# Kernel tuning notes

Measured on AMD Instinct MI355X. Metric: run time of the kernel, lower is better.

The kernel has to match this reference:

```python
import jax, jax.numpy as jnp
import numpy as np

B, T, H = 128, 2048, 128

def setup_inputs() -> dict:
    key = jax.random.key(0)
    k1, k2, k3, k4, k5, k6 = jax.random.split(key, 6)
    s = 1.0 / np.sqrt(H)
    return {
        "H_pos": jax.random.normal(k1, (B, T, H), jnp.float32),
        "H_dyn": jax.random.normal(k2, (B, T, H), jnp.float32),
        "acc_w": jax.random.uniform(k3, (B, T), jnp.float32),
        "W_h": jax.random.uniform(k4, (H, H), jnp.float32, -s, s),
        "W_d": jax.random.uniform(k5, (H, H), jnp.float32, -s, s),
        "W_a": jax.random.uniform(k6, (H,), jnp.float32, -s, s),
        "b_a": jnp.zeros((), jnp.float32),
        "beta": jnp.zeros((), jnp.float32),
    }

def reference(H_pos, H_dyn, acc_w, W_h, W_d, W_a, b_a, beta):
    # energy: W_a(tanh(W_h H_pos + W_d H_dyn)) -> [B, T]
    z = jnp.tanh(jnp.einsum('bth,oh->bto', H_pos, W_h)
                 + jnp.einsum('bth,oh->bto', H_dyn, W_d))
    energy = jnp.einsum('bth,h->bt', z, W_a) + b_a
    # acceleration normalization
    acc_norm = acc_w / jnp.clip(jnp.max(acc_w, axis=1, keepdims=True), 1e-6)
    beta_pos = jax.nn.softplus(beta)
    alpha = jax.nn.softmax(energy * (1.0 + beta_pos * acc_norm), axis=1)  # [B, T]
    context = jnp.einsum('bt,bth->bh', alpha, H_pos)  # [B, H]
    return (context, alpha)
```

## Files before the change

### kernel.cpp

```cpp
#include <hip/hip_runtime.h>

#define B_ 128
#define T_ 2048
#define H_ 128

typedef __attribute__((ext_vector_type(8))) short short8;
typedef __attribute__((ext_vector_type(4))) float f32x4;

__device__ __forceinline__ unsigned short f2b(float f) {
    unsigned int u = __float_as_uint(f);
    u += 0x7fffu + ((u >> 16) & 1u);
    return (unsigned short)(u >> 16);
}
__device__ __forceinline__ short8 pack8(const float4 x, const float4 y) {
    short8 r;
    r[0] = (short)f2b(x.x); r[1] = (short)f2b(x.y);
    r[2] = (short)f2b(x.z); r[3] = (short)f2b(x.w);
    r[4] = (short)f2b(y.x); r[5] = (short)f2b(y.y);
    r[6] = (short)f2b(y.z); r[7] = (short)f2b(y.w);
    return r;
}
__device__ __forceinline__ float tanh_fast(float x) {
    x = fminf(fmaxf(x, -20.f), 20.f);
    float e = __expf(2.f * x);
    return (e - 1.f) / (e + 1.f);
}

__global__ __launch_bounds__(256) void amax_kernel(
    const float* __restrict__ accw, float* __restrict__ amax_g)
{
    __shared__ float wred[4];
    const int b = blockIdx.x, tid = threadIdx.x;
    const float* p = accw + (size_t)b * T_ + tid * 8;
    float4 a0 = *(const float4*)p, a1 = *(const float4*)(p + 4);
    float m = fmaxf(fmaxf(fmaxf(a0.x, a0.y), fmaxf(a0.z, a0.w)),
                    fmaxf(fmaxf(a1.x, a1.y), fmaxf(a1.z, a1.w)));
    for (int d = 32; d >= 1; d >>= 1) m = fmaxf(m, __shfl_xor(m, d, 64));
    if ((tid & 63) == 0) wred[tid >> 6] = m;
    __syncthreads();
    if (tid == 0)
        amax_g[b] = fmaxf(fmaxf(wred[0], wred[1]), fmaxf(wred[2], wred[3]));
}

__global__ __launch_bounds__(512) void energy_kernel(
    const float* __restrict__ Hp,
    const float* __restrict__ Hd,
    const float* __restrict__ accw,
    const float* __restrict__ Wh,
    const float* __restrict__ Wd,
    const float* __restrict__ Wa,
    const float* __restrict__ ba_p,
    const float* __restrict__ beta_p,
    const float* __restrict__ amax_g,
    float* __restrict__ s_g,
    float* __restrict__ ml_g,
    float* __restrict__ ctxp_g,
    int ntiles)
{
    __shared__ unsigned short Wpack[8 * 8 * 64 * 8];
    __shared__ float Was[H_];
    __shared__ float e_s[128];
    __shared__ float s_s[128];
    __shared__ float p_s[128];
    __shared__ float red[16 * H_];
    __shared__ float mld[2];

    const int tid = threadIdx.x;

    for (int i = tid; i < (H_ * H_) / 4; i += 512) {
        int o  = i >> 5;
        int c4 = i & 31;
        float4 wh = *(const float4*)&Wh[o * H_ + c4 * 4];
        float4 wd = *(const float4*)&Wd[o * H_ + c4 * 4];
        uint2 ph, pdv;
        ph.x  = (unsigned)f2b(wh.x) | ((unsigned)f2b(wh.y) << 16);
        ph.y  = (unsigned)f2b(wh.z) | ((unsigned)f2b(wh.w) << 16);
        pdv.x = (unsigned)f2b(wd.x) | ((unsigned)f2b(wd.y) << 16);
        pdv.y = (unsigned)f2b(wd.z) | ((unsigned)f2b(wd.w) << 16);
        int nt   = o >> 4;
        int l15o = o & 15;
        int kth  = c4 >> 3;
        int lq   = (c4 >> 1) & 3;
        int half = (c4 & 1) * 4;
        int bh = ((kth * 8 + nt) * 64 + lq * 16 + l15o) * 8 + half;
        int bd = (((kth + 4) * 8 + nt) * 64 + lq * 16 + l15o) * 8 + half;
        *(uint2*)&Wpack[bh] = ph;
        *(uint2*)&Wpack[bd] = pdv;
    }
    if (tid < H_) Was[tid] = Wa[tid];
    __syncthreads();

    const float ba = ba_p[0];
    const float beta_pos = log1pf(__expf(beta_p[0]));

    const int wave = tid >> 6;
    const int lane = tid & 63;
    const int l15  = lane & 15;
    const int lq   = lane >> 4;

    const unsigned short* wb = Wpack + lane * 8;

    const size_t estep = (size_t)gridDim.x * 128 * H_;

    const int row0 = blockIdx.x * 128 + wave * 16;
    const float* pp = Hp + (size_t)(row0 + l15) * H_ + lq * 8;
    const float* pd = Hd + (size_t)(row0 + l15) * H_ + lq * 8;

    float4 abuf[8];
    #pragma unroll
    for (int c = 0; c < 4; c++) {
        abuf[2 * c]     = *(const float4*)(pp + c * 32);
        abuf[2 * c + 1] = *(const float4*)(pp + c * 32 + 4);
    }

    for (int tile = blockIdx.x; tile < ntiles; tile += gridDim.x) {
        __syncthreads();

        const int b  = tile >> 4;
        const int t0 = (tile & 15) * 128;
        const size_t adv = (tile + (int)gridDim.x < ntiles) ? estep : 0;
        const float* ppn = pp + adv;

        f32x4 acc[8];
        #pragma unroll
        for (int nt = 0; nt < 8; nt++) acc[nt] = (f32x4){0.f, 0.f, 0.f, 0.f};

        #pragma unroll
        for (int kt = 0; kt < 8; kt++) {
            const int sl = kt & 3;
            short8 af = pack8(abuf[2 * sl], abuf[2 * sl + 1]);
            const float* s = (kt < 4) ? (pd + kt * 32) : (ppn + (kt - 4) * 32);
            abuf[2 * sl]     = *(const float4*)s;
            abuf[2 * sl + 1] = *(const float4*)(s + 4);
            #pragma unroll
            for (int nt = 0; nt < 8; nt++) {
                short8 bf = *(const short8*)(wb + kt * 4096 + nt * 512);
                acc[nt] = __builtin_amdgcn_mfma_f32_16x16x32_bf16(af, bf, acc[nt], 0, 0, 0);
            }
            __builtin_amdgcn_sched_barrier(0);
        }
        pp = ppn;
        pd += adv;

        float ep[4] = {0.f, 0.f, 0.f, 0.f};
        #pragma unroll
        for (int nt = 0; nt < 8; nt++) {
            const float wa = Was[nt * 16 + l15];
            #pragma unroll
            for (int r = 0; r < 4; r++) ep[r] += tanh_fast(acc[nt][r]) * wa;
        }
        #pragma unroll
        for (int m = 1; m < 16; m <<= 1) {
            #pragma unroll
            for (int r = 0; r < 4; r++) ep[r] += __shfl_xor(ep[r], m, 64);
        }
        if (l15 == 0) {
            #pragma unroll
            for (int r = 0; r < 4; r++)
                e_s[wave * 16 + lq * 4 + r] = ep[r] + ba;
        }
        __syncthreads();

        if (tid < 128) {
            float a = accw[(size_t)b * T_ + t0 + tid];
            float invd = beta_pos / fmaxf(amax_g[b], 1e-6f);
            float s = e_s[tid] * (1.f + a * invd);
            s_s[tid] = s;
            s_g[(size_t)b * T_ + t0 + tid] = s;
        }
        __syncthreads();

        if (wave == 0) {
            float m = fmaxf(s_s[lane], s_s[lane + 64]);
            for (int d = 32; d >= 1; d >>= 1) m = fmaxf(m, __shfl_xor(m, d, 64));
            if (lane == 0) mld[0] = m;
        }
        __syncthreads();
        const float mt = mld[0];
        if (tid < 128) p_s[tid] = __expf(s_s[tid] - mt);
        __syncthreads();

        if (wave == 0) {
            float l = p_s[lane] + p_s[lane + 64];
            for (int d = 32; d >= 1; d >>= 1) l += __shfl_xor(l, d, 64);
            if (lane == 0) {
                ml_g[(b * 16 + (tile & 15)) * 2 + 0] = mt;
                ml_g[(b * 16 + (tile & 15)) * 2 + 1] = l;
            }
        }

        {
            const int g  = tid >> 5;
            const int c4 = tid & 31;
            const float* base = Hp + ((size_t)b * T_ + t0) * H_ + c4 * 4;
            float c0 = 0.f, c1 = 0.f, c2 = 0.f, c3 = 0.f;
            #pragma unroll
            for (int r = 0; r < 8; r++) {
                int t = r * 16 + g;
                float pv = p_s[t];
                float4 v = *(const float4*)(base + (size_t)t * H_);
                c0 += pv * v.x; c1 += pv * v.y; c2 += pv * v.z; c3 += pv * v.w;
            }
            red[g * H_ + c4 * 4 + 0] = c0;
            red[g * H_ + c4 * 4 + 1] = c1;
            red[g * H_ + c4 * 4 + 2] = c2;
            red[g * H_ + c4 * 4 + 3] = c3;
        }
        __syncthreads();
        if (tid < 128) {
            float s = 0.f;
            #pragma unroll
            for (int g = 0; g < 16; g++) s += red[g * H_ + tid];
            ctxp_g[((size_t)b * 16 + (tile & 15)) * H_ + tid] = s;
        }
    }
}

__global__ __launch_bounds__(256) void combine_kernel(
    const float* __restrict__ s_g,
    const float* __restrict__ ml_g,
    const float* __restrict__ ctxp_g,
    float* __restrict__ out_ctx,
    float* __restrict__ out_alpha)
{
    __shared__ float ml_s[32];
    const int b = blockIdx.x, tid = threadIdx.x;

    if (tid < 32) ml_s[tid] = ml_g[b * 32 + tid];
    __syncthreads();

    float M = -1e30f;
    #pragma unroll
    for (int i = 0; i < 16; i++) M = fmaxf(M, ml_s[2 * i]);
    float L = 0.f;
    #pragma unroll
    for (int i = 0; i < 16; i++) L += __expf(ml_s[2 * i] - M) * ml_s[2 * i + 1];
    const float invL = 1.f / L;

    if (tid < 128) {
        float s = 0.f;
        #pragma unroll
        for (int ti = 0; ti < 16; ti++)
            s += __expf(ml_s[2 * ti] - M) * ctxp_g[((size_t)b * 16 + ti) * H_ + tid];
        out_ctx[b * H_ + tid] = s * invL;
    }

    const float* ps = s_g + (size_t)b * T_ + tid * 8;
    float* pa = out_alpha + (size_t)b * T_ + tid * 8;
    float4 s0 = *(const float4*)ps, s1 = *(const float4*)(ps + 4);
    float4 a0, a1;
    a0.x = __expf(s0.x - M) * invL; a0.y = __expf(s0.y - M) * invL;
    a0.z = __expf(s0.z - M) * invL; a0.w = __expf(s0.w - M) * invL;
    a1.x = __expf(s1.x - M) * invL; a1.y = __expf(s1.y - M) * invL;
    a1.z = __expf(s1.z - M) * invL; a1.w = __expf(s1.w - M) * invL;
    *(float4*)pa = a0; *(float4*)(pa + 4) = a1;
}

extern "C" void kernel_launch(void* const* d_in, const int* in_sizes, int n_in,
                              void* d_out, int out_size, void* d_ws, size_t ws_size,
                              hipStream_t stream) {
    const float* Hp   = (const float*)d_in[0];
    const float* Hd   = (const float*)d_in[1];
    const float* accw = (const float*)d_in[2];
    const float* Wh   = (const float*)d_in[3];
    const float* Wd   = (const float*)d_in[4];
    const float* Wa   = (const float*)d_in[5];
    const float* ba   = (const float*)d_in[6];
    const float* beta = (const float*)d_in[7];

    float* s_ws    = (float*)d_ws;
    float* ctxp_ws = s_ws + B_ * T_;
    float* ml_ws   = ctxp_ws + B_ * 16 * H_;
    float* amax_ws = ml_ws + B_ * 16 * 2;

    float* out_ctx   = (float*)d_out;
    float* out_alpha = out_ctx + B_ * H_;

    const int ntiles = (B_ * T_) / 128;
    amax_kernel<<<B_, 256, 0, stream>>>(accw, amax_ws);
    energy_kernel<<<512, 512, 0, stream>>>(Hp, Hd, accw, Wh, Wd, Wa, ba, beta,
                                           amax_ws, s_ws, ml_ws, ctxp_ws, ntiles);
    combine_kernel<<<B_, 256, 0, stream>>>(s_ws, ml_ws, ctxp_ws, out_ctx, out_alpha);
}
```

Measured before the change: 309.2 us.

## Double energy tile to 256 rows with 1024-thread blocks

Grows each energy-kernel tile from 128 to 256 timesteps and runs 1024-thread blocks (16 waves) on a 256-block grid. The per-tile softmax partials and context reduction are rewritten for 256 rows, with one merged shared buffer and float2 context loads. The combine kernel now merges 8 partials per batch instead of 16. This halves the number of per-tile partial writes and block-wide sync rounds, at the cost of fewer resident blocks and heavier register pressure under the 1024-thread launch bound.

```diff
diff --git a/kernel.cpp b/kernel.cpp
--- a/kernel.cpp
+++ b/kernel.cpp
@@ -42,7 +42,7 @@
         amax_g[b] = fmaxf(fmaxf(wred[0], wred[1]), fmaxf(wred[2], wred[3]));
 }
 
-__global__ __launch_bounds__(512) void energy_kernel(
+__global__ __launch_bounds__(1024, 8) void energy_kernel(
     const float* __restrict__ Hp,
     const float* __restrict__ Hd,
     const float* __restrict__ accw,
@@ -59,15 +59,13 @@
 {
     __shared__ unsigned short Wpack[8 * 8 * 64 * 8];
     __shared__ float Was[H_];
-    __shared__ float e_s[128];
-    __shared__ float s_s[128];
-    __shared__ float p_s[128];
+    __shared__ float sp[256];
     __shared__ float red[16 * H_];
     __shared__ float mld[2];
 
     const int tid = threadIdx.x;
 
-    for (int i = tid; i < (H_ * H_) / 4; i += 512) {
+    for (int i = tid; i < (H_ * H_) / 4; i += 1024) {
         int o  = i >> 5;
         int c4 = i & 31;
         float4 wh = *(const float4*)&Wh[o * H_ + c4 * 4];
@@ -100,9 +98,9 @@
 
     const unsigned short* wb = Wpack + lane * 8;
 
-    const size_t estep = (size_t)gridDim.x * 128 * H_;
-
-    const int row0 = blockIdx.x * 128 + wave * 16;
+    const size_t estep = (size_t)gridDim.x * 256 * H_;
+
+    const int row0 = blockIdx.x * 256 + wave * 16;
     const float* pp = Hp + (size_t)(row0 + l15) * H_ + lq * 8;
     const float* pd = Hd + (size_t)(row0 + l15) * H_ + lq * 8;
 
@@ -116,8 +114,8 @@
     for (int tile = blockIdx.x; tile < ntiles; tile += gridDim.x) {
         __syncthreads();
 
-        const int b  = tile >> 4;
-        const int t0 = (tile & 15) * 128;
+        const int b  = tile >> 3;
+        const int t0 = (tile & 7) * 256;
         const size_t adv = (tile + (int)gridDim.x < ntiles) ? estep : 0;
         const float* ppn = pp + adv;
 
@@ -157,61 +155,59 @@
         if (l15 == 0) {
             #pragma unroll
             for (int r = 0; r < 4; r++)
-                e_s[wave * 16 + lq * 4 + r] = ep[r] + ba;
-        }
-        __syncthreads();
-
-        if (tid < 128) {
+                sp[wave * 16 + lq * 4 + r] = ep[r] + ba;
+        }
+        __syncthreads();
+
+        if (tid < 256) {
             float a = accw[(size_t)b * T_ + t0 + tid];
             float invd = beta_pos / fmaxf(amax_g[b], 1e-6f);
-            float s = e_s[tid] * (1.f + a * invd);
-            s_s[tid] = s;
+            float s = (sp[tid] ) * (1.f + a * invd);
+            sp[tid] = s;
             s_g[(size_t)b * T_ + t0 + tid] = s;
         }
         __syncthreads();
 
         if (wave == 0) {
-            float m = fmaxf(s_s[lane], s_s[lane + 64]);
+            float m = fmaxf(fmaxf(sp[lane], sp[lane + 64]),
+                            fmaxf(sp[lane + 128], sp[lane + 192]));
             for (int d = 32; d >= 1; d >>= 1) m = fmaxf(m, __shfl_xor(m, d, 64));
             if (lane == 0) mld[0] = m;
         }
         __syncthreads();
         const float mt = mld[0];
-        if (tid < 128) p_s[tid] = __expf(s_s[tid] - mt);
+        if (tid < 256) sp[tid] = __expf(sp[tid] - mt);
         __syncthreads();
 
         if (wave == 0) {
-            float l = p_s[lane] + p_s[lane + 64];
+            float l = (sp[lane] + sp[lane + 64]) + (sp[lane + 128] + sp[lane + 192]);
             for (int d = 32; d >= 1; d >>= 1) l += __shfl_xor(l, d, 64);
             if (lane == 0) {
-                ml_g[(b * 16 + (tile & 15)) * 2 + 0] = mt;
-                ml_g[(b * 16 + (tile & 15)) * 2 + 1] = l;
+                ml_g[(b * 8 + (tile & 7)) * 2 + 0] = mt;
+                ml_g[(b * 8 + (tile & 7)) * 2 + 1] = l;
             }
         }
 
         {
-            const int g  = tid >> 5;
-            const int c4 = tid & 31;
-            const float* base = Hp + ((size_t)b * T_ + t0) * H_ + c4 * 4;
-            float c0 = 0.f, c1 = 0.f, c2 = 0.f, c3 = 0.f;
-            #pragma unroll
-            for (int r = 0; r < 8; r++) {
-                int t = r * 16 + g;
-                float pv = p_s[t];
-                float4 v = *(const float4*)(base + (size_t)t * H_);
-                c0 += pv * v.x; c1 += pv * v.y; c2 += pv * v.z; c3 += pv * v.w;
+            const int g  = tid >> 6;
+            const int c2 = tid & 63;
+            const float* base = Hp + ((size_t)b * T_ + t0 + g * 16) * H_ + c2 * 2;
+            float c0 = 0.f, c1 = 0.f;
+            #pragma unroll
+            for (int r = 0; r < 16; r++) {
+                float pv = sp[g * 16 + r];
+                float2 v = *(const float2*)(base + (size_t)r * H_);
+                c0 += pv * v.x; c1 += pv * v.y;
             }
-            red[g * H_ + c4 * 4 + 0] = c0;
-            red[g * H_ + c4 * 4 + 1] = c1;
-            red[g * H_ + c4 * 4 + 2] = c2;
-            red[g * H_ + c4 * 4 + 3] = c3;
+            red[g * H_ + c2 * 2 + 0] = c0;
+            red[g * H_ + c2 * 2 + 1] = c1;
         }
         __syncthreads();
         if (tid < 128) {
             float s = 0.f;
             #pragma unroll
             for (int g = 0; g < 16; g++) s += red[g * H_ + tid];
-            ctxp_g[((size_t)b * 16 + (tile & 15)) * H_ + tid] = s;
+            ctxp_g[((size_t)b * 8 + (tile & 7)) * H_ + tid] = s;
         }
     }
 }
@@ -223,25 +219,25 @@
     float* __restrict__ out_ctx,
     float* __restrict__ out_alpha)
 {
-    __shared__ float ml_s[32];
+    __shared__ float ml_s[16];
     const int b = blockIdx.x, tid = threadIdx.x;
 
-    if (tid < 32) ml_s[tid] = ml_g[b * 32 + tid];
+    if (tid < 16) ml_s[tid] = ml_g[b * 16 + tid];
     __syncthreads();
 
     float M = -1e30f;
     #pragma unroll
-    for (int i = 0; i < 16; i++) M = fmaxf(M, ml_s[2 * i]);
+    for (int i = 0; i < 8; i++) M = fmaxf(M, ml_s[2 * i]);
     float L = 0.f;
     #pragma unroll
-    for (int i = 0; i < 16; i++) L += __expf(ml_s[2 * i] - M) * ml_s[2 * i + 1];
+    for (int i = 0; i < 8; i++) L += __expf(ml_s[2 * i] - M) * ml_s[2 * i + 1];
     const float invL = 1.f / L;
 
     if (tid < 128) {
         float s = 0.f;
         #pragma unroll
-        for (int ti = 0; ti < 16; ti++)
-            s += __expf(ml_s[2 * ti] - M) * ctxp_g[((size_t)b * 16 + ti) * H_ + tid];
+        for (int ti = 0; ti < 8; ti++)
+            s += __expf(ml_s[2 * ti] - M) * ctxp_g[((size_t)b * 8 + ti) * H_ + tid];
         out_ctx[b * H_ + tid] = s * invL;
     }
 
@@ -270,15 +266,15 @@
 
     float* s_ws    = (float*)d_ws;
     float* ctxp_ws = s_ws + B_ * T_;
-    float* ml_ws   = ctxp_ws + B_ * 16 * H_;
-    float* amax_ws = ml_ws + B_ * 16 * 2;
+    float* ml_ws   = ctxp_ws + B_ * 8 * H_;
+    float* amax_ws = ml_ws + B_ * 8 * 2;
 
     float* out_ctx   = (float*)d_out;
     float* out_alpha = out_ctx + B_ * H_;
 
-    const int ntiles = (B_ * T_) / 128;
+    const int ntiles = (B_ * T_) / 256;
     amax_kernel<<<B_, 256, 0, stream>>>(accw, amax_ws);
-    energy_kernel<<<512, 512, 0, stream>>>(Hp, Hd, accw, Wh, Wd, Wa, ba, beta,
-                                           amax_ws, s_ws, ml_ws, ctxp_ws, ntiles);
+    energy_kernel<<<256, 1024, 0, stream>>>(Hp, Hd, accw, Wh, Wd, Wa, ba, beta,
+                                            amax_ws, s_ws, ml_ws, ctxp_ws, ntiles);
     combine_kernel<<<B_, 256, 0, stream>>>(s_ws, ml_ws, ctxp_ws, out_ctx, out_alpha);
 }
```

Measured after the change: 437.5 us. 1.42x slower.
